# Optimization experiments

Measured on AMD Instinct MI355X. Metric: run time of the kernel, lower is better.

Reference implementation:

```python
import jax, jax.numpy as jnp
import numpy as np

N = 96
M = 96
# visual field constants
L_V_EX, S_V_EX, L_V_IN, S_V_IN = 1.6, 3.5, 1.23, 6.3
FV, TAU_V, UPS_V, P_V, K_V = 1.0, 3.0, 3.0, 0.3, 7.0
# auditory field constants
L_A_EX, S_A_EX, L_A_IN, S_A_IN = 1.0, 5.3, 0.8, 11.8
FA, TAU_A, UPS_A, P_A, K_A = 1.0, 3.0, 3.0, 0.3, 3.0
# multisensory field constants
L_M_EX, S_M_EX, L_M_IN, S_M_IN = 3.8, 3.5, 3.3, 6.2
TAU_M, UPS_M, P_M = 3.0, 3.0, 0.3


def _torus_sqdist():
    # squared toroidal distance components: dx2[i,h], dy2[j,k]
    ii = jnp.arange(N, dtype=jnp.float32)
    jj = jnp.arange(M, dtype=jnp.float32)
    dx = jnp.abs(ii[:, None] - ii[None, :])
    dx = jnp.minimum(dx, N - dx)
    dy = jnp.abs(jj[:, None] - jj[None, :])
    dy = jnp.minimum(dy, M - dy)
    # aux[i,j,h,k] = dx[i,h]^2 + dy[j,k]^2
    return dx[:, None, :, None] ** 2 + dy[None, :, None, :] ** 2


def _dog(aux, l_ex, s_ex, l_in, s_in):
    # Faithful to source: exp(-aux/2 * sigma**2) == exp(-0.5*aux*sigma^2)
    return l_ex * jnp.exp(-0.5 * aux * (s_ex ** 2)) - l_in * jnp.exp(-0.5 * aux * (s_in ** 2))


def setup_inputs() -> dict:
    key = jax.random.key(0)
    ks = jax.random.split(key, 7)
    return {
        "video": jax.random.normal(ks[0], (32, 1024), dtype=jnp.float32),
        "audio": jax.random.normal(ks[1], (32, 2048), dtype=jnp.float32),
        "rf_v": jax.random.normal(ks[2], (N, M, 1024), dtype=jnp.float32) * (1.0 / np.sqrt(1024.0)),
        "rf_a": jax.random.normal(ks[3], (N, M, 2048), dtype=jnp.float32) * (1.0 / np.sqrt(2048.0)),
        "na_v": jax.random.normal(ks[4], (N, M), dtype=jnp.float32),
        "na_a": jax.random.normal(ks[5], (N, M), dtype=jnp.float32),
        "na_m": jax.random.normal(ks[6], (N, M), dtype=jnp.float32),
    }


def reference(video, audio, rf_v, rf_a, na_v, na_a, na_m):
    aux = _torus_sqdist()  # (N, M, N, M)
    syn_v = _dog(aux, L_V_EX, S_V_EX, L_V_IN, S_V_IN)
    syn_a = _dog(aux, L_A_EX, S_A_EX, L_A_IN, S_A_IN)
    syn_m = _dog(aux, L_M_EX, S_M_EX, L_M_IN, S_M_IN)

    # external inputs: sum over feature dim -> (B, N, M)
    ext_v = jnp.einsum('bv,ijv->bij', video, rf_v)
    ext_a = jnp.einsum('ba,ija->bij', audio, rf_a)

    # all-pairs neighbor inputs: neighbor[i,j] = sum_{h,k} act[h,k] * syn[i,j,h,k]
    nb_v = jnp.einsum('ijhk,hk->ij', syn_v, na_v)
    nb_a = jnp.einsum('ijhk,hk->ij', syn_a, na_a)

    coll_v = FV * na_m
    coll_a = FA * na_m

    na_v_new = na_v * (TAU_V - 1.0) / TAU_V + (1.0 / TAU_V) * jax.nn.sigmoid(
        (ext_v + nb_v - UPS_V + coll_v) * P_V)  # (B, N, M)
    na_a_new = na_a * (TAU_A - 1.0) / TAU_A + (1.0 / TAU_A) * jax.nn.sigmoid(
        (ext_a + nb_a - UPS_A + coll_a) * P_A)  # (B, N, M)

    nb_m = jnp.einsum('ijhk,hk->ij', syn_m, na_m)
    na_m_new = na_m * (TAU_M - 1.0) / TAU_M + (1.0 / TAU_M) * jax.nn.sigmoid(
        (K_V * na_v_new + K_A * na_a_new + nb_m - UPS_M) * P_M)  # (B, N, M)
    return na_m_new
```

## Files before the change

### kernel.cpp

```cpp
#include <hip/hip_runtime.h>
#include <math.h>

#define NN   96
#define NPOS (96*96)
#define BB   32
#define KV   1024
#define KA   2048
#define KCH  256
#define NCHV (KV/KCH)
#define NCHA (KA/KCH)
#define POSB 64
#define PBLK (NPOS/POSB)
#define NBLK_V (NCHV*PBLK)
#define NBLK_A (NCHA*PBLK)

#define PARTV_OFF 0
#define PARTA_OFF (NCHV*BB*NPOS)
#define CPT_OFF   (PARTA_OFF + NCHA*BB*NPOS)
#define AFV_OFF   (CPT_OFF + 6*NPOS)
#define AFV_SLOTS ((KV/32)*2*64)
#define AFA_OFF   (AFV_OFF + AFV_SLOTS*4)
#define AFA_SLOTS ((KA/32)*2*64)

typedef __bf16 bf16x8 __attribute__((ext_vector_type(8)));
typedef float  f32x4  __attribute__((ext_vector_type(4)));

__global__ __launch_bounds__(256) void nbT_kernel(
    const float* __restrict__ na_v, const float* __restrict__ na_a,
    const float* __restrict__ na_m, const float* __restrict__ video,
    const float* __restrict__ audio, float* __restrict__ ws)
{
    __shared__ float G[96][100];
    __shared__ float act_s[96][100];
    __shared__ float T1t[24][100];

    if (blockIdx.x >= 24) {
        const int e = (blockIdx.x - 24) * 256 + threadIdx.x;
        const float* src; bf16x8* dst; int K, el;
        if (e < AFV_SLOTS) { src = video; K = KV; dst = (bf16x8*)(ws + AFV_OFF); el = e; }
        else               { src = audio; K = KA; dst = (bf16x8*)(ws + AFA_OFF); el = e - AFV_SLOTS; }
        const int l  = el & 63;
        const int hb = (el >> 6) & 1;
        const int sg = el >> 7;
        const int b  = hb * 16 + (l & 15);
        const int k0 = sg * 32 + ((l >> 4) << 3);
        const float4 f0 = *(const float4*)&src[(size_t)b * K + k0];
        const float4 f1 = *(const float4*)&src[(size_t)b * K + k0 + 4];
        bf16x8 v;
        v[0] = (__bf16)f0.x; v[1] = (__bf16)f0.y; v[2] = (__bf16)f0.z; v[3] = (__bf16)f0.w;
        v[4] = (__bf16)f1.x; v[5] = (__bf16)f1.y; v[6] = (__bf16)f1.z; v[7] = (__bf16)f1.w;
        dst[el] = v;
        return;
    }

    const int c  = blockIdx.x >> 2;
    const int js = (blockIdx.x & 3) * 24;
    float l, s;
    if      (c == 0) { l =  1.60f; s = 3.5f;  }
    else if (c == 1) { l = -1.23f; s = 6.3f;  }
    else if (c == 2) { l =  1.00f; s = 5.3f;  }
    else if (c == 3) { l = -0.80f; s = 11.8f; }
    else if (c == 4) { l =  3.80f; s = 3.5f;  }
    else             { l = -3.30f; s = 6.2f;  }
    const float s2 = s * s;
    const int f = c >> 1;
    const float* act = (f == 0) ? na_v : (f == 1) ? na_a : na_m;
    const int tid = threadIdx.x;
    float* cpt = ws + CPT_OFF;

    for (int idx = tid; idx < 9216; idx += 256) {
        int j = idx / 96, k = idx - j * 96;
        int d = abs(j - k); d = min(d, 96 - d);
        G[j][k]     = __expf(-0.5f * (float)(d * d) * s2);
        act_s[j][k] = act[idx];
    }
    __syncthreads();

    const int hg3 = (tid >> 3) * 3;
    const int jl3 = (tid & 7) * 3;

    float t1[3][3] = {};
    for (int k0 = 0; k0 < 96; k0 += 4) {
        float4 av[3], gv[3];
        #pragma unroll
        for (int r = 0; r < 3; r++) {
            av[r] = *(const float4*)&act_s[hg3 + r][k0];
            gv[r] = *(const float4*)&G[js + jl3 + r][k0];
        }
        #pragma unroll
        for (int hh = 0; hh < 3; hh++)
            #pragma unroll
            for (int jj = 0; jj < 3; jj++)
                t1[hh][jj] += av[hh].x * gv[jj].x + av[hh].y * gv[jj].y
                            + av[hh].z * gv[jj].z + av[hh].w * gv[jj].w;
    }
    #pragma unroll
    for (int hh = 0; hh < 3; hh++)
        #pragma unroll
        for (int jj = 0; jj < 3; jj++)
            T1t[jl3 + jj][hg3 + hh] = t1[hh][jj];
    __syncthreads();

    float o[3][3] = {};
    for (int h0 = 0; h0 < 96; h0 += 4) {
        float4 gv[3], tv[3];
        #pragma unroll
        for (int r = 0; r < 3; r++) {
            gv[r] = *(const float4*)&G[hg3 + r][h0];
            tv[r] = *(const float4*)&T1t[jl3 + r][h0];
        }
        #pragma unroll
        for (int ii = 0; ii < 3; ii++)
            #pragma unroll
            for (int jj = 0; jj < 3; jj++)
                o[ii][jj] += gv[ii].x * tv[jj].x + gv[ii].y * tv[jj].y
                           + gv[ii].z * tv[jj].z + gv[ii].w * tv[jj].w;
    }
    #pragma unroll
    for (int ii = 0; ii < 3; ii++)
        #pragma unroll
        for (int jj = 0; jj < 3; jj++)
            cpt[c * NPOS + (hg3 + ii) * 96 + (js + jl3 + jj)] = l * o[ii][jj];
}

__global__ __launch_bounds__(256, 6) void ext_mfma(
    const float* __restrict__ rf_v, const float* __restrict__ rf_a,
    float* __restrict__ ws)
{
    const int bid = blockIdx.x;
    const float* rf; const bf16x8* af; float* part; int K;
    int chunk, pt;
    if (bid < NBLK_V) {
        chunk = bid / PBLK; pt = bid - chunk * PBLK;
        rf = rf_v; K = KV;
        af = (const bf16x8*)(ws + AFV_OFF);
        part = ws + PARTV_OFF + (size_t)chunk * (BB * NPOS);
    } else {
        const int idx = bid - NBLK_V;
        chunk = idx / PBLK; pt = idx - chunk * PBLK;
        rf = rf_a; K = KA;
        af = (const bf16x8*)(ws + AFA_OFF);
        part = ws + PARTA_OFF + (size_t)chunk * (BB * NPOS);
    }
    const int kbase = chunk * KCH;
    const int l  = threadIdx.x & 63;
    const int p0 = pt * POSB + (threadIdx.x >> 6) * 16;
    const int prow = p0 + (l & 15);
    const int koff = (l >> 4) * 8;
    const float4* bp = (const float4*)(rf + (size_t)prow * K + kbase + koff);
    const bf16x8* ap = af + (kbase >> 5) * 128 + l;

    f32x4 acc0 = {0.f, 0.f, 0.f, 0.f};
    f32x4 acc1 = {0.f, 0.f, 0.f, 0.f};

    #pragma unroll
    for (int st = 0; st < KCH / 32; ++st) {
        bf16x8 a0 = ap[st * 128];
        bf16x8 a1 = ap[st * 128 + 64];
        float4 f0 = bp[st * 8];
        float4 f1 = bp[st * 8 + 1];
        bf16x8 bv;
        bv[0] = (__bf16)f0.x; bv[1] = (__bf16)f0.y; bv[2] = (__bf16)f0.z; bv[3] = (__bf16)f0.w;
        bv[4] = (__bf16)f1.x; bv[5] = (__bf16)f1.y; bv[6] = (__bf16)f1.z; bv[7] = (__bf16)f1.w;
        acc0 = __builtin_amdgcn_mfma_f32_16x16x32_bf16(a0, bv, acc0, 0, 0, 0);
        acc1 = __builtin_amdgcn_mfma_f32_16x16x32_bf16(a1, bv, acc1, 0, 0, 0);
    }

    const int pcol  = p0 + (l & 15);
    const int brow0 = (l >> 4) * 4;
    #pragma unroll
    for (int r = 0; r < 4; ++r) {
        part[(size_t)(brow0 + r) * NPOS + pcol]      = acc0[r];
        part[(size_t)(16 + brow0 + r) * NPOS + pcol] = acc1[r];
    }
}

__global__ __launch_bounds__(256) void combine_kernel(
    const float* __restrict__ na_v, const float* __restrict__ na_a,
    const float* __restrict__ na_m, const float* __restrict__ ws,
    float* __restrict__ out)
{
    const int npq = NPOS >> 2;
    const int t = blockIdx.x * 256 + threadIdx.x;
    if (t >= BB * npq) return;
    const int b  = t / npq;
    const int p0 = (t - b * npq) << 2;

    float4 ev = {0.f, 0.f, 0.f, 0.f}, ea = {0.f, 0.f, 0.f, 0.f};
    #pragma unroll
    for (int c = 0; c < NCHV; c++) {
        float4 x = *(const float4*)&ws[PARTV_OFF + (size_t)c * (BB * NPOS) + (size_t)b * NPOS + p0];
        ev.x += x.x; ev.y += x.y; ev.z += x.z; ev.w += x.w;
    }
    #pragma unroll
    for (int c = 0; c < NCHA; c++) {
        float4 x = *(const float4*)&ws[PARTA_OFF + (size_t)c * (BB * NPOS) + (size_t)b * NPOS + p0];
        ea.x += x.x; ea.y += x.y; ea.z += x.z; ea.w += x.w;
    }
    const float* cpt = ws + CPT_OFF;
    float4 q0 = *(const float4*)&cpt[0 * NPOS + p0];
    float4 q1 = *(const float4*)&cpt[1 * NPOS + p0];
    float4 q2 = *(const float4*)&cpt[2 * NPOS + p0];
    float4 q3 = *(const float4*)&cpt[3 * NPOS + p0];
    float4 q4 = *(const float4*)&cpt[4 * NPOS + p0];
    float4 q5 = *(const float4*)&cpt[5 * NPOS + p0];
    float4 nv = *(const float4*)&na_v[p0];
    float4 na = *(const float4*)&na_a[p0];
    float4 nm = *(const float4*)&na_m[p0];

    float evs[4] = {ev.x, ev.y, ev.z, ev.w};
    float eas[4] = {ea.x, ea.y, ea.z, ea.w};
    float nbv[4] = {q0.x + q1.x, q0.y + q1.y, q0.z + q1.z, q0.w + q1.w};
    float nba[4] = {q2.x + q3.x, q2.y + q3.y, q2.z + q3.z, q2.w + q3.w};
    float nbm[4] = {q4.x + q5.x, q4.y + q5.y, q4.z + q5.z, q4.w + q5.w};
    float nvs[4] = {nv.x, nv.y, nv.z, nv.w};
    float nas[4] = {na.x, na.y, na.z, na.w};
    float nms[4] = {nm.x, nm.y, nm.z, nm.w};

    float4 o;
    float* os = (float*)&o;
    #pragma unroll
    for (int u = 0; u < 4; u++) {
        const float xv = (evs[u] + nbv[u] - 3.0f + nms[u]) * 0.3f;
        const float nav_new = nvs[u] * (2.f / 3.f) + (1.f / 3.f) / (1.f + __expf(-xv));
        const float xa = (eas[u] + nba[u] - 3.0f + nms[u]) * 0.3f;
        const float naa_new = nas[u] * (2.f / 3.f) + (1.f / 3.f) / (1.f + __expf(-xa));
        const float xm = (7.0f * nav_new + 3.0f * naa_new + nbm[u] - 3.0f) * 0.3f;
        os[u] = nms[u] * (2.f / 3.f) + (1.f / 3.f) / (1.f + __expf(-xm));
    }
    *(float4*)&out[(size_t)b * NPOS + p0] = o;
}

extern "C" void kernel_launch(void* const* d_in, const int* in_sizes, int n_in,
                              void* d_out, int out_size, void* d_ws, size_t ws_size,
                              hipStream_t stream) {
    const float* video = (const float*)d_in[0];
    const float* audio = (const float*)d_in[1];
    const float* rf_v  = (const float*)d_in[2];
    const float* rf_a  = (const float*)d_in[3];
    const float* na_v  = (const float*)d_in[4];
    const float* na_a  = (const float*)d_in[5];
    const float* na_m  = (const float*)d_in[6];
    float* ws  = (float*)d_ws;
    float* out = (float*)d_out;

    nbT_kernel<<<72, 256, 0, stream>>>(na_v, na_a, na_m, video, audio, ws);
    ext_mfma<<<NBLK_V + NBLK_A, 256, 0, stream>>>(rf_v, rf_a, ws);
    combine_kernel<<<(BB * NPOS / 4 + 255) / 256, 256, 0, stream>>>(
        na_v, na_a, na_m, ws, out);
}
```

Before: 42.88 us.

## Replace K-split partial sums with full-K LDS-pipelined MFMA loop per position tile

Each block now covers 32 positions over the whole K range instead of one 256-wide K chunk. A 4-stage global_load_lds ring with XOR-swizzled LDS feeds the bf16 MFMA, and barriers plus vmcnt waits control the pipeline. This drops the partial-sum buffers and the reduction reads in the combine kernel. The cost is fewer, longer blocks (576 instead of 1728), audio blocks running twice as long as video ones, and a barrier per K step, so the load may balance worse.

```diff
diff --git a/kernel.cpp b/kernel.cpp
--- a/kernel.cpp
+++ b/kernel.cpp
@@ -6,20 +6,15 @@
 #define BB   32
 #define KV   1024
 #define KA   2048
-#define KCH  256
-#define NCHV (KV/KCH)
-#define NCHA (KA/KCH)
-#define POSB 64
+#define POSB 32
 #define PBLK (NPOS/POSB)
-#define NBLK_V (NCHV*PBLK)
-#define NBLK_A (NCHA*PBLK)
-
-#define PARTV_OFF 0
-#define PARTA_OFF (NCHV*BB*NPOS)
-#define CPT_OFF   (PARTA_OFF + NCHA*BB*NPOS)
-#define AFV_OFF   (CPT_OFF + 6*NPOS)
+
+#define EXTV_OFF 0
+#define EXTA_OFF (BB*NPOS)
+#define CPT_OFF  (2*BB*NPOS)
+#define AFV_OFF  (CPT_OFF + 6*NPOS)
 #define AFV_SLOTS ((KV/32)*2*64)
-#define AFA_OFF   (AFV_OFF + AFV_SLOTS*4)
+#define AFA_OFF  (AFV_OFF + AFV_SLOTS*4)
 #define AFA_SLOTS ((KA/32)*2*64)
 
 typedef __bf16 bf16x8 __attribute__((ext_vector_type(8)));
@@ -123,56 +118,82 @@
             cpt[c * NPOS + (hg3 + ii) * 96 + (js + jl3 + jj)] = l * o[ii][jj];
 }
 
-__global__ __launch_bounds__(256, 6) void ext_mfma(
+__global__ __launch_bounds__(256) void ext_mfma(
     const float* __restrict__ rf_v, const float* __restrict__ rf_a,
     float* __restrict__ ws)
 {
+    __shared__ float lds[4 * 1536];
     const int bid = blockIdx.x;
-    const float* rf; const bf16x8* af; float* part; int K;
-    int chunk, pt;
-    if (bid < NBLK_V) {
-        chunk = bid / PBLK; pt = bid - chunk * PBLK;
-        rf = rf_v; K = KV;
-        af = (const bf16x8*)(ws + AFV_OFF);
-        part = ws + PARTV_OFF + (size_t)chunk * (BB * NPOS);
+    const float* rf; const bf16x8* af; float* ext; int K, NS, pt;
+    if (bid < PBLK) {
+        pt = bid; rf = rf_a; K = KA; NS = KA / 32;
+        af  = (const bf16x8*)(ws + AFA_OFF);
+        ext = ws + EXTA_OFF;
     } else {
-        const int idx = bid - NBLK_V;
-        chunk = idx / PBLK; pt = idx - chunk * PBLK;
-        rf = rf_a; K = KA;
-        af = (const bf16x8*)(ws + AFA_OFF);
-        part = ws + PARTA_OFF + (size_t)chunk * (BB * NPOS);
-    }
-    const int kbase = chunk * KCH;
-    const int l  = threadIdx.x & 63;
-    const int p0 = pt * POSB + (threadIdx.x >> 6) * 16;
-    const int prow = p0 + (l & 15);
-    const int koff = (l >> 4) * 8;
-    const float4* bp = (const float4*)(rf + (size_t)prow * K + kbase + koff);
-    const bf16x8* ap = af + (kbase >> 5) * 128 + l;
-
-    f32x4 acc0 = {0.f, 0.f, 0.f, 0.f};
-    f32x4 acc1 = {0.f, 0.f, 0.f, 0.f};
-
-    #pragma unroll
-    for (int st = 0; st < KCH / 32; ++st) {
-        bf16x8 a0 = ap[st * 128];
-        bf16x8 a1 = ap[st * 128 + 64];
-        float4 f0 = bp[st * 8];
-        float4 f1 = bp[st * 8 + 1];
+        pt = bid - PBLK; rf = rf_v; K = KV; NS = KV / 32;
+        af  = (const bf16x8*)(ws + AFV_OFF);
+        ext = ws + EXTV_OFF;
+    }
+    const int tid = threadIdx.x;
+    const int l  = tid & 63, w = tid >> 6;
+    const int ph = w & 1, bh = w >> 1;
+
+    const int srow = w * 8 + (l >> 3);
+    const int kc   = (l & 7) ^ ((l >> 3) & 7);
+    const float*  gsrc0 = rf + (size_t)(pt * 32 + srow) * K + kc * 4;
+    const bf16x8* asrc0 = af + (w & 1) * 64 + l;
+
+    char* ldsc = (char*)lds;
+    const int rf_dst = w * 1024;
+    const int af_dst = 4096 + (w & 1) * 1024;
+
+    const int rrow  = ph * 16 + (l & 15);
+    const int c0    = (l >> 4) * 2;
+    const int roff0 = rrow * 128 + ((c0       ^ (rrow & 7)) * 16);
+    const int roff1 = rrow * 128 + (((c0 + 1) ^ (rrow & 7)) * 16);
+    const int aoff  = 4096 + bh * 1024 + l * 16;
+
+#define STAGE(tt, dd)                                                         \
+    do {                                                                      \
+        const int t_ = (tt) < NS ? (tt) : NS - 1;                             \
+        __builtin_amdgcn_global_load_lds(                                     \
+            (const __attribute__((address_space(1))) void*)(gsrc0 + t_ * 32), \
+            (__attribute__((address_space(3))) void*)(ldsc + (dd) * 6144 + rf_dst), \
+            16, 0, 0);                                                        \
+        __builtin_amdgcn_global_load_lds(                                     \
+            (const __attribute__((address_space(1))) void*)(asrc0 + t_ * 128),\
+            (__attribute__((address_space(3))) void*)(ldsc + (dd) * 6144 + af_dst), \
+            16, 0, 0);                                                        \
+    } while (0)
+
+    STAGE(0, 0); STAGE(1, 1); STAGE(2, 2); STAGE(3, 3);
+
+    f32x4 acc = {0.f, 0.f, 0.f, 0.f};
+    for (int t = 0; t < NS; ++t) {
+        const int d = t & 3;
+        const char* buf = ldsc + d * 6144;
+        asm volatile("s_waitcnt vmcnt(6)" ::: "memory");
+        __builtin_amdgcn_s_barrier();
+        __builtin_amdgcn_sched_barrier(0);
+        f32x4  b0 = *(const f32x4*)(buf + roff0);
+        f32x4  b1 = *(const f32x4*)(buf + roff1);
+        bf16x8 av = *(const bf16x8*)(buf + aoff);
         bf16x8 bv;
-        bv[0] = (__bf16)f0.x; bv[1] = (__bf16)f0.y; bv[2] = (__bf16)f0.z; bv[3] = (__bf16)f0.w;
-        bv[4] = (__bf16)f1.x; bv[5] = (__bf16)f1.y; bv[6] = (__bf16)f1.z; bv[7] = (__bf16)f1.w;
-        acc0 = __builtin_amdgcn_mfma_f32_16x16x32_bf16(a0, bv, acc0, 0, 0, 0);
-        acc1 = __builtin_amdgcn_mfma_f32_16x16x32_bf16(a1, bv, acc1, 0, 0, 0);
-    }
-
-    const int pcol  = p0 + (l & 15);
-    const int brow0 = (l >> 4) * 4;
-    #pragma unroll
-    for (int r = 0; r < 4; ++r) {
-        part[(size_t)(brow0 + r) * NPOS + pcol]      = acc0[r];
-        part[(size_t)(16 + brow0 + r) * NPOS + pcol] = acc1[r];
-    }
+        bv[0] = (__bf16)b0[0]; bv[1] = (__bf16)b0[1]; bv[2] = (__bf16)b0[2]; bv[3] = (__bf16)b0[3];
+        bv[4] = (__bf16)b1[0]; bv[5] = (__bf16)b1[1]; bv[6] = (__bf16)b1[2]; bv[7] = (__bf16)b1[3];
+        acc = __builtin_amdgcn_mfma_f32_16x16x32_bf16(av, bv, acc, 0, 0, 0);
+        __builtin_amdgcn_sched_barrier(0);
+        __builtin_amdgcn_s_barrier();
+        __builtin_amdgcn_sched_barrier(0);
+        STAGE(t + 4, d);
+    }
+#undef STAGE
+
+    const int pcol  = pt * 32 + ph * 16 + (l & 15);
+    const int brow0 = bh * 16 + (l >> 4) * 4;
+    #pragma unroll
+    for (int r = 0; r < 4; ++r)
+        ext[(size_t)(brow0 + r) * NPOS + pcol] = acc[r];
 }
 
 __global__ __launch_bounds__(256) void combine_kernel(
@@ -186,17 +207,8 @@
     const int b  = t / npq;
     const int p0 = (t - b * npq) << 2;
 
-    float4 ev = {0.f, 0.f, 0.f, 0.f}, ea = {0.f, 0.f, 0.f, 0.f};
-    #pragma unroll
-    for (int c = 0; c < NCHV; c++) {
-        float4 x = *(const float4*)&ws[PARTV_OFF + (size_t)c * (BB * NPOS) + (size_t)b * NPOS + p0];
-        ev.x += x.x; ev.y += x.y; ev.z += x.z; ev.w += x.w;
-    }
-    #pragma unroll
-    for (int c = 0; c < NCHA; c++) {
-        float4 x = *(const float4*)&ws[PARTA_OFF + (size_t)c * (BB * NPOS) + (size_t)b * NPOS + p0];
-        ea.x += x.x; ea.y += x.y; ea.z += x.z; ea.w += x.w;
-    }
+    float4 ev = *(const float4*)&ws[EXTV_OFF + (size_t)b * NPOS + p0];
+    float4 ea = *(const float4*)&ws[EXTA_OFF + (size_t)b * NPOS + p0];
     const float* cpt = ws + CPT_OFF;
     float4 q0 = *(const float4*)&cpt[0 * NPOS + p0];
     float4 q1 = *(const float4*)&cpt[1 * NPOS + p0];
@@ -245,7 +257,7 @@
     float* out = (float*)d_out;
 
     nbT_kernel<<<72, 256, 0, stream>>>(na_v, na_a, na_m, video, audio, ws);
-    ext_mfma<<<NBLK_V + NBLK_A, 256, 0, stream>>>(rf_v, rf_a, ws);
+    ext_mfma<<<2 * PBLK, 256, 0, stream>>>(rf_v, rf_a, ws);
     combine_kernel<<<(BB * NPOS / 4 + 255) / 256, 256, 0, stream>>>(
         na_v, na_a, na_m, ws, out);
 }
```

Measured after the change: 47.38 us. +10.5%, slower.

## Restructure ext GEMM with LDS-staged rf tiles and in-block K reduction

Applied to the files above, without the earlier changes.

Each block in the ext GEMM now covers 16 positions over a K span of 1024. It loads the rf rows with coalesced float4 reads, converts them to bf16 and stages them in shared memory. The MFMA loop then reads B fragments from LDS, and two wave groups split K and reduce through LDS. This replaces the previous 256-wide K chunks, which produced 12 partial buffers that combine_kernel had to sum, so partial-sum global writes and reads drop sharply. In exchange the kernel adds shared memory use, two barriers and a lower occupancy bound.

```diff
diff --git a/kernel.cpp b/kernel.cpp
--- a/kernel.cpp
+++ b/kernel.cpp
@@ -6,23 +6,18 @@
 #define BB   32
 #define KV   1024
 #define KA   2048
-#define KCH  256
-#define NCHV (KV/KCH)
-#define NCHA (KA/KCH)
-#define POSB 64
-#define PBLK (NPOS/POSB)
-#define NBLK_V (NCHV*PBLK)
-#define NBLK_A (NCHA*PBLK)
-
-#define PARTV_OFF 0
-#define PARTA_OFF (NCHV*BB*NPOS)
-#define CPT_OFF   (PARTA_OFF + NCHA*BB*NPOS)
+
+#define EXTV_OFF  0
+#define EXTA0_OFF (BB*NPOS)
+#define EXTA1_OFF (2*BB*NPOS)
+#define CPT_OFF   (3*BB*NPOS)
 #define AFV_OFF   (CPT_OFF + 6*NPOS)
 #define AFV_SLOTS ((KV/32)*2*64)
 #define AFA_OFF   (AFV_OFF + AFV_SLOTS*4)
 #define AFA_SLOTS ((KA/32)*2*64)
 
 typedef __bf16 bf16x8 __attribute__((ext_vector_type(8)));
+typedef __bf16 bf16x4 __attribute__((ext_vector_type(4)));
 typedef float  f32x4  __attribute__((ext_vector_type(4)));
 
 __global__ __launch_bounds__(256) void nbT_kernel(
@@ -123,55 +118,73 @@
             cpt[c * NPOS + (hg3 + ii) * 96 + (js + jl3 + jj)] = l * o[ii][jj];
 }
 
-__global__ __launch_bounds__(256, 6) void ext_mfma(
+#define LDS_ROW 2064
+__global__ __launch_bounds__(256, 4) void ext_mfma(
     const float* __restrict__ rf_v, const float* __restrict__ rf_a,
     float* __restrict__ ws)
 {
+    __shared__ char lds[16 * LDS_ROW + 2048];
+    const int tid = threadIdx.x;
     const int bid = blockIdx.x;
-    const float* rf; const bf16x8* af; float* part; int K;
-    int chunk, pt;
-    if (bid < NBLK_V) {
-        chunk = bid / PBLK; pt = bid - chunk * PBLK;
-        rf = rf_v; K = KV;
-        af = (const bf16x8*)(ws + AFV_OFF);
-        part = ws + PARTV_OFF + (size_t)chunk * (BB * NPOS);
+
+    const float* rf; const bf16x8* af; float* ext; int K, kb, pt;
+    if (bid < 1152) {
+        const int c = bid / 576; pt = bid - c * 576;
+        rf = rf_a; K = KA; kb = c << 10;
+        af  = (const bf16x8*)(ws + AFA_OFF);
+        ext = ws + EXTA0_OFF + c * (BB * NPOS);
     } else {
-        const int idx = bid - NBLK_V;
-        chunk = idx / PBLK; pt = idx - chunk * PBLK;
-        rf = rf_a; K = KA;
-        af = (const bf16x8*)(ws + AFA_OFF);
-        part = ws + PARTA_OFF + (size_t)chunk * (BB * NPOS);
-    }
-    const int kbase = chunk * KCH;
-    const int l  = threadIdx.x & 63;
-    const int p0 = pt * POSB + (threadIdx.x >> 6) * 16;
-    const int prow = p0 + (l & 15);
-    const int koff = (l >> 4) * 8;
-    const float4* bp = (const float4*)(rf + (size_t)prow * K + kbase + koff);
-    const bf16x8* ap = af + (kbase >> 5) * 128 + l;
-
-    f32x4 acc0 = {0.f, 0.f, 0.f, 0.f};
-    f32x4 acc1 = {0.f, 0.f, 0.f, 0.f};
-
-    #pragma unroll
-    for (int st = 0; st < KCH / 32; ++st) {
-        bf16x8 a0 = ap[st * 128];
-        bf16x8 a1 = ap[st * 128 + 64];
-        float4 f0 = bp[st * 8];
-        float4 f1 = bp[st * 8 + 1];
-        bf16x8 bv;
-        bv[0] = (__bf16)f0.x; bv[1] = (__bf16)f0.y; bv[2] = (__bf16)f0.z; bv[3] = (__bf16)f0.w;
-        bv[4] = (__bf16)f1.x; bv[5] = (__bf16)f1.y; bv[6] = (__bf16)f1.z; bv[7] = (__bf16)f1.w;
-        acc0 = __builtin_amdgcn_mfma_f32_16x16x32_bf16(a0, bv, acc0, 0, 0, 0);
-        acc1 = __builtin_amdgcn_mfma_f32_16x16x32_bf16(a1, bv, acc1, 0, 0, 0);
-    }
-
-    const int pcol  = p0 + (l & 15);
-    const int brow0 = (l >> 4) * 4;
-    #pragma unroll
-    for (int r = 0; r < 4; ++r) {
-        part[(size_t)(brow0 + r) * NPOS + pcol]      = acc0[r];
-        part[(size_t)(16 + brow0 + r) * NPOS + pcol] = acc1[r];
+        pt = bid - 1152; rf = rf_v; K = KV; kb = 0;
+        af  = (const bf16x8*)(ws + AFV_OFF);
+        ext = ws + EXTV_OFF;
+    }
+
+    {
+        const float* src = rf + (size_t)(pt * 16) * K + kb + tid * 4;
+        float4 fa[8];
+        #pragma unroll
+        for (int j = 0; j < 8; ++j) fa[j] = *(const float4*)(src + (size_t)j * K);
+        #pragma unroll
+        for (int j = 0; j < 8; ++j) {
+            bf16x4 v;
+            v[0] = (__bf16)fa[j].x; v[1] = (__bf16)fa[j].y;
+            v[2] = (__bf16)fa[j].z; v[3] = (__bf16)fa[j].w;
+            *(bf16x4*)(lds + j * LDS_ROW + tid * 8) = v;
+        }
+        #pragma unroll
+        for (int j = 0; j < 8; ++j) fa[j] = *(const float4*)(src + (size_t)(j + 8) * K);
+        #pragma unroll
+        for (int j = 0; j < 8; ++j) {
+            bf16x4 v;
+            v[0] = (__bf16)fa[j].x; v[1] = (__bf16)fa[j].y;
+            v[2] = (__bf16)fa[j].z; v[3] = (__bf16)fa[j].w;
+            *(bf16x4*)(lds + (j + 8) * LDS_ROW + tid * 8) = v;
+        }
+    }
+    __syncthreads();
+
+    const int l  = tid & 63, w = tid >> 6;
+    const int bh = w & 1, kh = w >> 1;
+    const bf16x8* ap = af + ((kb >> 5) + (kh << 4)) * 128 + (bh << 6) + l;
+    const char*   bp = lds + (l & 15) * LDS_ROW + (kh << 10) + ((l >> 4) << 4);
+    f32x4 acc = {0.f, 0.f, 0.f, 0.f};
+    #pragma unroll
+    for (int s = 0; s < 16; ++s) {
+        bf16x8 a = ap[s * 128];
+        bf16x8 b = *(const bf16x8*)(bp + s * 64);
+        acc = __builtin_amdgcn_mfma_f32_16x16x32_bf16(a, b, acc, 0, 0, 0);
+    }
+
+    if (kh) *(f32x4*)(lds + 16 * LDS_ROW + (bh << 10) + l * 16) = acc;
+    __syncthreads();
+    if (!kh) {
+        f32x4 o = *(const f32x4*)(lds + 16 * LDS_ROW + (bh << 10) + l * 16);
+        acc += o;
+        const int pcol = pt * 16 + (l & 15);
+        const int br0  = (bh << 4) + ((l >> 4) << 2);
+        #pragma unroll
+        for (int r = 0; r < 4; ++r)
+            ext[(size_t)(br0 + r) * NPOS + pcol] = acc[r];
     }
 }
 
@@ -186,17 +199,10 @@
     const int b  = t / npq;
     const int p0 = (t - b * npq) << 2;
 
-    float4 ev = {0.f, 0.f, 0.f, 0.f}, ea = {0.f, 0.f, 0.f, 0.f};
-    #pragma unroll
-    for (int c = 0; c < NCHV; c++) {
-        float4 x = *(const float4*)&ws[PARTV_OFF + (size_t)c * (BB * NPOS) + (size_t)b * NPOS + p0];
-        ev.x += x.x; ev.y += x.y; ev.z += x.z; ev.w += x.w;
-    }
-    #pragma unroll
-    for (int c = 0; c < NCHA; c++) {
-        float4 x = *(const float4*)&ws[PARTA_OFF + (size_t)c * (BB * NPOS) + (size_t)b * NPOS + p0];
-        ea.x += x.x; ea.y += x.y; ea.z += x.z; ea.w += x.w;
-    }
+    float4 ev  = *(const float4*)&ws[EXTV_OFF  + (size_t)b * NPOS + p0];
+    float4 ea0 = *(const float4*)&ws[EXTA0_OFF + (size_t)b * NPOS + p0];
+    float4 ea1 = *(const float4*)&ws[EXTA1_OFF + (size_t)b * NPOS + p0];
+    float4 ea = {ea0.x + ea1.x, ea0.y + ea1.y, ea0.z + ea1.z, ea0.w + ea1.w};
     const float* cpt = ws + CPT_OFF;
     float4 q0 = *(const float4*)&cpt[0 * NPOS + p0];
     float4 q1 = *(const float4*)&cpt[1 * NPOS + p0];
@@ -245,7 +251,7 @@
     float* out = (float*)d_out;
 
     nbT_kernel<<<72, 256, 0, stream>>>(na_v, na_a, na_m, video, audio, ws);
-    ext_mfma<<<NBLK_V + NBLK_A, 256, 0, stream>>>(rf_v, rf_a, ws);
+    ext_mfma<<<1728, 256, 0, stream>>>(rf_v, rf_a, ws);
     combine_kernel<<<(BB * NPOS / 4 + 255) / 256, 256, 0, stream>>>(
         na_v, na_a, na_m, ws, out);
 }
```

Measured after the change: 37.83 us (median of 3 runs). -11.8%, faster.
